# Kernel tuning notes

Hardware: AMD Instinct MI355X
Metric: run time of the kernel (lower is better)

## Reference

```python
import jax, jax.numpy as jnp
import numpy as np

POLY_DEGREE = 3


def setup_inputs() -> dict:
    key = jax.random.key(0)
    k1, k2, k3 = jax.random.split(key, 3)
    B, L, D = 8192, 16, 4096
    total = sum(L ** d for d in range(POLY_DEGREE + 1))  # 4369
    z = jax.random.normal(k1, (B, L), dtype=jnp.float32)
    W = jax.random.normal(k2, (total, D), dtype=jnp.float32) * 0.02
    b = jax.random.normal(k3, (D,), dtype=jnp.float32) * 0.02
    return {"z": z, "W": W, "b": b}


def poly_features(z):
    # Batched equivalent of per-sample torch.kron chain:
    # degree 0 -> [1]; degree k -> kron(deg_{k-1} feature, z) per sample.
    B = z.shape[0]
    feats = [jnp.ones((B, 1), dtype=z.dtype)]
    cur = z  # degree 1
    feats.append(cur)
    for _ in range(2, POLY_DEGREE + 1):
        # kron(out, latent): (i, j) -> out_i * latent_j
        cur = (cur[:, :, None] * z[:, None, :]).reshape(B, -1)
        feats.append(cur)
    return jnp.concatenate(feats, axis=1)  # [B, total_poly_terms]


def reference(z, W, b):
    x = poly_features(z)          # [B, T]
    return x @ W + b              # [B, data_dim]
```

## Files before the change

kernel.cpp:

```cpp
#include <hip/hip_runtime.h>
#include <hip/hip_bf16.h>

#define NDIM  4096
#define MROWS 8192
#define PREAL 969
#define KP    1024
#define NT    16
#define NWFOLD 1024

typedef unsigned short u16;
typedef __attribute__((ext_vector_type(8))) __bf16 bf16x8;
typedef __attribute__((ext_vector_type(8))) u16 u16x8;
typedef __attribute__((ext_vector_type(4))) float f32x4;

__device__ __forceinline__ u16 bf16rne(float f) {
  unsigned int u = __builtin_bit_cast(unsigned int, f);
  u += 0x7fffu + ((u >> 16) & 1u);
  return (u16)(u >> 16);
}

struct Tbl { int v[KP]; };
constexpr Tbl make_table() {
  Tbl t{};
  for (int p = 0; p < KP; ++p) t.v[p] = -1;
  int p = 0;
  t.v[p++] = (16 << 10) | (16 << 5) | 16;
  for (int i = 0; i < 16; ++i) t.v[p++] = (i << 10) | (16 << 5) | 16;
  for (int i = 0; i < 16; ++i)
    for (int j = i; j < 16; ++j) t.v[p++] = (i << 10) | (j << 5) | 16;
  for (int i = 0; i < 16; ++i)
    for (int j = i; j < 16; ++j)
      for (int k = j; k < 16; ++k) t.v[p++] = (i << 10) | (j << 5) | k;
  return t;
}
__device__ constexpr Tbl TBL = make_table();

__global__ void prep_kernel(const float* __restrict__ z, const float* __restrict__ W,
                            const float* __restrict__ bias,
                            u16* __restrict__ xb, u16* __restrict__ wfbt) {
  __shared__ float tile[64][65];
  __shared__ float zs[17];
  const int bx = blockIdx.x;
  const int tid = threadIdx.x;

  if (bx < NWFOLD) {
    const int p0 = (bx & 15) * 64;
    const int d0 = (bx >> 4) * 64;
    const int d4 = (tid & 15) * 4;
    const int rb = tid >> 4;
    const int dd = d0 + d4;
#pragma unroll
    for (int pp = 0; pp < 4; ++pp) {
      const int r = pp * 16 + rb;
      const int p = p0 + r;
      const int enc = TBL.v[p];
      f32x4 v = {0.f, 0.f, 0.f, 0.f};
      if (enc >= 0) {
        const int i = enc >> 10, j = (enc >> 5) & 31, k = enc & 31;
        if (k == 16) {
          if (j == 16) {
            if (i == 16) {
              v = *reinterpret_cast<const f32x4*>(W + dd);
              f32x4 bb = *reinterpret_cast<const f32x4*>(bias + dd);
              v.x += bb.x; v.y += bb.y; v.z += bb.z; v.w += bb.w;
            } else {
              v = *reinterpret_cast<const f32x4*>(W + (size_t)(1 + i) * NDIM + dd);
            }
          } else {
            v = *reinterpret_cast<const f32x4*>(W + (size_t)(17 + i * 16 + j) * NDIM + dd);
            if (i != j) {
              f32x4 w2 = *reinterpret_cast<const f32x4*>(W + (size_t)(17 + j * 16 + i) * NDIM + dd);
              v.x += w2.x; v.y += w2.y; v.z += w2.z; v.w += w2.w;
            }
          }
        } else {
          int rows[6];
          int nr = 0;
          rows[nr++] = 273 + i * 256 + j * 16 + k;
          if (i == j && j == k) {
          } else if (i == j) {
            rows[nr++] = 273 + i * 256 + k * 16 + i;
            rows[nr++] = 273 + k * 256 + i * 16 + i;
          } else if (j == k) {
            rows[nr++] = 273 + j * 256 + i * 16 + j;
            rows[nr++] = 273 + j * 256 + j * 16 + i;
          } else {
            rows[nr++] = 273 + i * 256 + k * 16 + j;
            rows[nr++] = 273 + j * 256 + i * 16 + k;
            rows[nr++] = 273 + j * 256 + k * 16 + i;
            rows[nr++] = 273 + k * 256 + i * 16 + j;
            rows[nr++] = 273 + k * 256 + j * 16 + i;
          }
          v = *reinterpret_cast<const f32x4*>(W + (size_t)rows[0] * NDIM + dd);
          for (int s = 1; s < nr; ++s) {
            f32x4 w2 = *reinterpret_cast<const f32x4*>(W + (size_t)rows[s] * NDIM + dd);
            v.x += w2.x; v.y += w2.y; v.z += w2.z; v.w += w2.w;
          }
        }
      }
#pragma unroll
      for (int jj = 0; jj < 4; ++jj) tile[r][d4 + jj] = v[jj];
    }
    __syncthreads();
#pragma unroll
    for (int round = 0; round < 2; ++round) {
      const int v = round * 256 + tid;
      const int d = v >> 3;
      const int tg = v & 7;
      u16x8 pack;
#pragma unroll
      for (int e = 0; e < 8; ++e) pack[e] = bf16rne(tile[tg * 8 + e][d]);
      *reinterpret_cast<u16x8*>(wfbt + (size_t)(d0 + d) * KP + p0 + tg * 8) = pack;
    }
  } else {
    const int row = bx - NWFOLD;
    if (tid < 16) zs[tid] = z[row * 16 + tid];
    if (tid == 16) zs[16] = 1.0f;
    __syncthreads();
    u16* xrow = xb + (size_t)row * KP;
    for (int g = tid; g < KP / 8; g += 256) {
      u16x8 pack;
#pragma unroll
      for (int e = 0; e < 8; ++e) {
        const int enc = TBL.v[g * 8 + e];
        float v = 0.0f;
        if (enc >= 0) v = zs[enc >> 10] * (zs[(enc >> 5) & 31] * zs[enc & 31]);
        pack[e] = bf16rne(v);
      }
      *reinterpret_cast<u16x8*>(xrow + g * 8) = pack;
    }
  }
}

#define GLOAD(gp, lp)                                                                     \
  __builtin_amdgcn_global_load_lds((const __attribute__((address_space(1))) unsigned int*)(gp), \
                                   (__attribute__((address_space(3))) unsigned int*)(lp), 16, 0, 0)

__device__ __forceinline__ void bar() {
  asm volatile("" ::: "memory");
  __builtin_amdgcn_s_barrier();
  asm volatile("" ::: "memory");
}

#define VM4 asm volatile("s_waitcnt vmcnt(4)" ::: "memory")

__global__ __launch_bounds__(512, 2) void gemm_kernel(const u16* __restrict__ xb,
                                                      const u16* __restrict__ wbt,
                                                      float* __restrict__ out) {
  __shared__ u16 lds[2 * 32768];

  const int bid  = blockIdx.x;
  const int xcd  = bid & 7;
  const int idx  = bid >> 3;
  const int mtl  = (idx >> 3) & 3;
  const int ntl  = (idx & 7) | ((idx >> 5) << 3);
  const int brow = (xcd * 4 + mtl) * 256;
  const int bcol = ntl * 256;

  const int tid  = threadIdx.x;
  const int lane = tid & 63;
  const int wid  = tid >> 6;
  const int wr   = wid >> 2;
  const int wc   = wid & 3;
  const int f    = lane & 15;
  const int q    = lane >> 4;
  const int f7   = f & 7;

  const int lr = lane >> 3;
  const int swzc = ((lane & 7) ^ lr) * 8;
  const u16* gA = xb  + (size_t)(brow + lr) * KP + swzc;
  const u16* gB = wbt + (size_t)(bcol + lr) * KP + swzc;
  const int aB0 = (wid >> 2) * 128 + (wid & 3) * 16;
  const int bB0 = (wid >> 1) * 64 + (wid & 1) * 16;

#define STGQ(gptr, region, rb, U) do {                                               \
    GLOAD((gptr) + (size_t)(rb) * KP + (U) * 64, (region) + (rb) * 64);              \
    GLOAD((gptr) + (size_t)((rb) + 8) * KP + (U) * 64, (region) + ((rb) + 8) * 64);  \
  } while (0)

#define RD_A(mi, kk) (*reinterpret_cast<const bf16x8*>(bufA + (wr * 128 + (mi) * 16 + f) * 64 + (((kk) * 4 + q) ^ f7) * 8))
#define RD_B(ni, kk) (*reinterpret_cast<const bf16x8*>(bufB + (wc * 64 + (ni) * 16 + f) * 64 + (((kk) * 4 + q) ^ f7) * 8))

#define RDA4(MOFF) do {                                                              \
    _Pragma("unroll") for (int _i = 0; _i < 4; ++_i) {                               \
      a_[_i][0] = RD_A((MOFF) + _i, 0); a_[_i][1] = RD_A((MOFF) + _i, 1); }          \
  } while (0)
#define RDB2(NOFF) do {                                                              \
    _Pragma("unroll") for (int _i = 0; _i < 2; ++_i) {                               \
      b_[(NOFF) + _i][0] = RD_B((NOFF) + _i, 0); b_[(NOFF) + _i][1] = RD_B((NOFF) + _i, 1); } \
  } while (0)

#define QUAD(MOFF, NOFF) do {                                                        \
    __builtin_amdgcn_s_setprio(1);                                                   \
    _Pragma("unroll") for (int _m = 0; _m < 4; ++_m)                                 \
    _Pragma("unroll") for (int _n = 0; _n < 2; ++_n)                                 \
    _Pragma("unroll") for (int _k = 0; _k < 2; ++_k)                                 \
      acc[(MOFF) + _m][(NOFF) + _n] = __builtin_amdgcn_mfma_f32_16x16x32_bf16(       \
          a_[_m][_k], b_[(NOFF) + _n][_k], acc[(MOFF) + _m][(NOFF) + _n], 0, 0, 0);  \
    __builtin_amdgcn_s_setprio(0);                                                   \
  } while (0)

#define TILE_BODY(cA, cB, nA, nB, U) do {                                            \
    bufA = (cA); bufB = (cB);                                                        \
    RDA4(0); RDB2(0); STGQ(gA, (nA), aB0, (U));                                      \
    bar(); QUAD(0, 0); VM4; bar();                                                   \
    RDB2(2);          STGQ(gB, (nB), bB0, (U));                                      \
    bar(); QUAD(0, 2); VM4; bar();                                                   \
    RDA4(4);          STGQ(gB, (nB), bB0 + 32, (U));                                 \
    bar(); QUAD(4, 2); bar();                                                        \
                      STGQ(gA, (nA), aB0 + 64, (U));                                 \
    bar(); QUAD(4, 0); VM4; bar();                                                   \
  } while (0)

  f32x4 acc[8][4] = {};
  bf16x8 a_[4][2], b_[4][2];
  const u16 *bufA, *bufB;

  u16* b0A = lds;            u16* b0B = lds + 16384;
  u16* b1A = lds + 32768;    u16* b1B = b1A + 16384;

  STGQ(gA, b0A, aB0, 0); STGQ(gB, b0B, bB0, 0);
  STGQ(gB, b0B, bB0 + 32, 0); STGQ(gA, b0A, aB0 + 64, 0);
  VM4; bar();

  for (int t = 0; t < NT; t += 2) {
    const int u2 = (t + 2 < NT) ? (t + 2) : 0;
    TILE_BODY(b0A, b0B, b1A, b1B, t + 1);
    TILE_BODY(b1A, b1B, b0A, b0B, u2);
  }
  asm volatile("s_waitcnt vmcnt(0)" ::: "memory");

  const int r0 = brow + wr * 128 + q * 4;
  const int c0 = bcol + wc * 64 + f;
#pragma unroll
  for (int mi = 0; mi < 8; ++mi)
#pragma unroll
    for (int ni = 0; ni < 4; ++ni) {
#pragma unroll
      for (int j = 0; j < 4; ++j)
        out[(size_t)(r0 + mi * 16 + j) * NDIM + (c0 + ni * 16)] = acc[mi][ni][j];
    }
}

__global__ void fallback_kernel(const float* __restrict__ z, const float* __restrict__ W,
                                const float* __restrict__ bias, float* __restrict__ out) {
  __shared__ float feat[4369];
  const int row = blockIdx.x;
  const int tid = threadIdx.x;
  for (int t = tid; t < 4369; t += 256) {
    float v;
    if (t == 0) v = 1.0f;
    else if (t < 17) v = z[row * 16 + t - 1];
    else if (t < 273) { int u = t - 17; v = z[row * 16 + (u >> 4)] * z[row * 16 + (u & 15)]; }
    else { int u = t - 273; v = z[row * 16 + ((u >> 8) & 15)] * (z[row * 16 + ((u >> 4) & 15)] * z[row * 16 + (u & 15)]); }
    feat[t] = v;
  }
  __syncthreads();
  float acc[16];
#pragma unroll
  for (int j = 0; j < 16; ++j) acc[j] = bias[tid + 256 * j];
  for (int t = 0; t < 4369; ++t) {
    const float fv = feat[t];
    const float* wrow = W + (size_t)t * NDIM;
#pragma unroll
    for (int j = 0; j < 16; ++j) acc[j] = fmaf(fv, wrow[tid + 256 * j], acc[j]);
  }
  float* orow = out + (size_t)row * NDIM;
#pragma unroll
  for (int j = 0; j < 16; ++j) orow[tid + 256 * j] = acc[j];
}

extern "C" void kernel_launch(void* const* d_in, const int* in_sizes, int n_in,
                              void* d_out, int out_size, void* d_ws, size_t ws_size,
                              hipStream_t stream) {
  const float* z = (const float*)d_in[0];
  const float* W = (const float*)d_in[1];
  const float* b = (const float*)d_in[2];
  float* out = (float*)d_out;

  const size_t xb_elems  = (size_t)MROWS * KP;
  const size_t wbt_elems = (size_t)NDIM * KP;
  const size_t need = (xb_elems + wbt_elems) * sizeof(u16);

  if (ws_size >= need) {
    u16* xb  = (u16*)d_ws;
    u16* wbt = xb + xb_elems;
    prep_kernel<<<NWFOLD + MROWS, 256, 0, stream>>>(z, W, b, xb, wbt);
    gemm_kernel<<<(MROWS / 256) * (NDIM / 256), 512, 0, stream>>>(xb, wbt, out);
  } else {
    fallback_kernel<<<MROWS, 256, 0, stream>>>(z, W, b, out);
  }
}
```

Measured before the change: 104.3 us.

## Process two N-tiles per block to overlap epilogue stores with next tile's prefetch

Each GEMM block now computes two adjacent 256-column output tiles in sequence, halving the grid to 256 blocks. The first K-loop's last stage prefetches the second tile's B data, so the pipeline keeps loading while the first tile's results are written. Output stores become nontemporal, and a dedicated last-tile body drains outstanding loads with smaller waitcnts. The grid shrinks to exactly one wave of 256 blocks, which cuts tail effects but lowers total parallelism and changes the XCD mapping.

```diff
diff --git a/kernel.cpp b/kernel.cpp
--- a/kernel.cpp
+++ b/kernel.cpp
@@ -143,6 +143,8 @@
 }
 
 #define VM4 asm volatile("s_waitcnt vmcnt(4)" ::: "memory")
+#define VM2 asm volatile("s_waitcnt vmcnt(2)" ::: "memory")
+#define VM0 asm volatile("s_waitcnt vmcnt(0)" ::: "memory")
 
 __global__ __launch_bounds__(512, 2) void gemm_kernel(const u16* __restrict__ xb,
                                                       const u16* __restrict__ wbt,
@@ -152,10 +154,10 @@
   const int bid  = blockIdx.x;
   const int xcd  = bid & 7;
   const int idx  = bid >> 3;
-  const int mtl  = (idx >> 3) & 3;
-  const int ntl  = (idx & 7) | ((idx >> 5) << 3);
+  const int mtl  = idx >> 3;
+  const int npr  = idx & 7;
   const int brow = (xcd * 4 + mtl) * 256;
-  const int bcol = ntl * 256;
+  const int bcol = npr * 512;
 
   const int tid  = threadIdx.x;
   const int lane = tid & 63;
@@ -168,8 +170,9 @@
 
   const int lr = lane >> 3;
   const int swzc = ((lane & 7) ^ lr) * 8;
-  const u16* gA = xb  + (size_t)(brow + lr) * KP + swzc;
-  const u16* gB = wbt + (size_t)(bcol + lr) * KP + swzc;
+  const u16* gA  = xb  + (size_t)(brow + lr) * KP + swzc;
+  const u16* gB  = wbt + (size_t)(bcol + lr) * KP + swzc;
+  const u16* gB2 = gB + (size_t)256 * KP;
   const int aB0 = (wid >> 2) * 128 + (wid & 3) * 16;
   const int bB0 = (wid >> 1) * 64 + (wid & 1) * 16;
 
@@ -200,18 +203,29 @@
     __builtin_amdgcn_s_setprio(0);                                                   \
   } while (0)
 
-#define TILE_BODY(cA, cB, nA, nB, U) do {                                            \
+#define TILE_BODY(cA, cB, nA, nB, U, GBP) do {                                       \
     bufA = (cA); bufB = (cB);                                                        \
     RDA4(0); RDB2(0); STGQ(gA, (nA), aB0, (U));                                      \
     bar(); QUAD(0, 0); VM4; bar();                                                   \
-    RDB2(2);          STGQ(gB, (nB), bB0, (U));                                      \
+    RDB2(2);          STGQ((GBP), (nB), bB0, (U));                                   \
     bar(); QUAD(0, 2); VM4; bar();                                                   \
-    RDA4(4);          STGQ(gB, (nB), bB0 + 32, (U));                                 \
+    RDA4(4);          STGQ((GBP), (nB), bB0 + 32, (U));                              \
     bar(); QUAD(4, 2); bar();                                                        \
                       STGQ(gA, (nA), aB0 + 64, (U));                                 \
     bar(); QUAD(4, 0); VM4; bar();                                                   \
   } while (0)
 
+#define TILE_LAST(cA, cB) do {                                                       \
+    bufA = (cA); bufB = (cB);                                                        \
+    RDA4(0); RDB2(0);                                                                \
+    bar(); QUAD(0, 0); VM2; bar();                                                   \
+    RDB2(2);                                                                         \
+    bar(); QUAD(0, 2); VM0; bar();                                                   \
+    RDA4(4);                                                                         \
+    bar(); QUAD(4, 2); bar();                                                        \
+    QUAD(4, 0);                                                                      \
+  } while (0)
+
   f32x4 acc[8][4] = {};
   bf16x8 a_[4][2], b_[4][2];
   const u16 *bufA, *bufB;
@@ -223,23 +237,54 @@
   STGQ(gB, b0B, bB0 + 32, 0); STGQ(gA, b0A, aB0 + 64, 0);
   VM4; bar();
 
-  for (int t = 0; t < NT; t += 2) {
-    const int u2 = (t + 2 < NT) ? (t + 2) : 0;
-    TILE_BODY(b0A, b0B, b1A, b1B, t + 1);
-    TILE_BODY(b1A, b1B, b0A, b0B, u2);
-  }
-  asm volatile("s_waitcnt vmcnt(0)" ::: "memory");
-
-  const int r0 = brow + wr * 128 + q * 4;
-  const int c0 = bcol + wc * 64 + f;
+  for (int t = 0; t < NT - 2; t += 2) {
+    TILE_BODY(b0A, b0B, b1A, b1B, t + 1, gB);
+    TILE_BODY(b1A, b1B, b0A, b0B, t + 2, gB);
+  }
+  TILE_BODY(b0A, b0B, b1A, b1B, NT - 1, gB);
+  TILE_BODY(b1A, b1B, b0A, b0B, 0, gB2);
+
+  {
+    const int r0 = brow + wr * 128 + q * 4;
+    const int c0 = bcol + wc * 64 + f;
+#pragma unroll
+    for (int mi = 0; mi < 8; ++mi)
+#pragma unroll
+      for (int ni = 0; ni < 4; ++ni)
+#pragma unroll
+        for (int j = 0; j < 4; ++j)
+          __builtin_nontemporal_store(acc[mi][ni][j],
+              &out[(size_t)(r0 + mi * 16 + j) * NDIM + (c0 + ni * 16)]);
+  }
+  VM0; bar();
+
 #pragma unroll
   for (int mi = 0; mi < 8; ++mi)
 #pragma unroll
     for (int ni = 0; ni < 4; ++ni) {
-#pragma unroll
-      for (int j = 0; j < 4; ++j)
-        out[(size_t)(r0 + mi * 16 + j) * NDIM + (c0 + ni * 16)] = acc[mi][ni][j];
+      const f32x4 z4 = {0.f, 0.f, 0.f, 0.f};
+      acc[mi][ni] = z4;
     }
+
+  for (int t = 0; t < NT - 2; t += 2) {
+    TILE_BODY(b0A, b0B, b1A, b1B, t + 1, gB2);
+    TILE_BODY(b1A, b1B, b0A, b0B, t + 2, gB2);
+  }
+  TILE_BODY(b0A, b0B, b1A, b1B, NT - 1, gB2);
+  TILE_LAST(b1A, b1B);
+
+  {
+    const int r0 = brow + wr * 128 + q * 4;
+    const int c0 = bcol + 256 + wc * 64 + f;
+#pragma unroll
+    for (int mi = 0; mi < 8; ++mi)
+#pragma unroll
+      for (int ni = 0; ni < 4; ++ni)
+#pragma unroll
+        for (int j = 0; j < 4; ++j)
+          __builtin_nontemporal_store(acc[mi][ni][j],
+              &out[(size_t)(r0 + mi * 16 + j) * NDIM + (c0 + ni * 16)]);
+  }
 }
 
 __global__ void fallback_kernel(const float* __restrict__ z, const float* __restrict__ W,
@@ -286,7 +331,7 @@
     u16* xb  = (u16*)d_ws;
     u16* wbt = xb + xb_elems;
     prep_kernel<<<NWFOLD + MROWS, 256, 0, stream>>>(z, W, b, xb, wbt);
-    gemm_kernel<<<(MROWS / 256) * (NDIM / 256), 512, 0, stream>>>(xb, wbt, out);
+    gemm_kernel<<<(MROWS / 256) * (NDIM / 512), 512, 0, stream>>>(xb, wbt, out);
   } else {
     fallback_kernel<<<MROWS, 256, 0, stream>>>(z, W, b, out);
   }
```

After: 139.8 us. 1.34x slower.

## Software-pipeline LDS fragment reads against MFMA quads across tile boundaries

Applied to the files above, without the earlier changes.

Restructures the GEMM main loop so each quad of MFMAs uses fragments loaded in the previous phase, while the next phase's LDS reads are issued first. The last quad of a tile is deferred into the next tile, with a peeled prologue and epilogue. About half the barriers per tile are removed. The goal is to hide LDS read latency behind matrix-core work, at the cost of more live fragment registers (double-buffered A and B) and possible spills at the 2-waves occupancy bound.

```diff
diff --git a/kernel.cpp b/kernel.cpp
--- a/kernel.cpp
+++ b/kernel.cpp
@@ -143,6 +143,8 @@
 }
 
 #define VM4 asm volatile("s_waitcnt vmcnt(4)" ::: "memory")
+#define VM1 asm volatile("s_waitcnt vmcnt(1)" ::: "memory")
+#define VM0 asm volatile("s_waitcnt vmcnt(0)" ::: "memory")
 
 __global__ __launch_bounds__(512, 2) void gemm_kernel(const u16* __restrict__ xb,
                                                       const u16* __restrict__ wbt,
@@ -181,39 +183,39 @@
 #define RD_A(mi, kk) (*reinterpret_cast<const bf16x8*>(bufA + (wr * 128 + (mi) * 16 + f) * 64 + (((kk) * 4 + q) ^ f7) * 8))
 #define RD_B(ni, kk) (*reinterpret_cast<const bf16x8*>(bufB + (wc * 64 + (ni) * 16 + f) * 64 + (((kk) * 4 + q) ^ f7) * 8))
 
-#define RDA4(MOFF) do {                                                              \
+#define RDA_TO(DST, MOFF) do {                                                       \
     _Pragma("unroll") for (int _i = 0; _i < 4; ++_i) {                               \
-      a_[_i][0] = RD_A((MOFF) + _i, 0); a_[_i][1] = RD_A((MOFF) + _i, 1); }          \
-  } while (0)
-#define RDB2(NOFF) do {                                                              \
+      DST[_i][0] = RD_A((MOFF) + _i, 0); DST[_i][1] = RD_A((MOFF) + _i, 1); }        \
+  } while (0)
+#define RDB_TO(DST, NOFF) do {                                                       \
     _Pragma("unroll") for (int _i = 0; _i < 2; ++_i) {                               \
-      b_[(NOFF) + _i][0] = RD_B((NOFF) + _i, 0); b_[(NOFF) + _i][1] = RD_B((NOFF) + _i, 1); } \
-  } while (0)
-
-#define QUAD(MOFF, NOFF) do {                                                        \
+      DST[_i][0] = RD_B((NOFF) + _i, 0); DST[_i][1] = RD_B((NOFF) + _i, 1); }        \
+  } while (0)
+
+#define QUADX(MOFF, NOFF, AF, BF) do {                                               \
     __builtin_amdgcn_s_setprio(1);                                                   \
     _Pragma("unroll") for (int _m = 0; _m < 4; ++_m)                                 \
     _Pragma("unroll") for (int _n = 0; _n < 2; ++_n)                                 \
     _Pragma("unroll") for (int _k = 0; _k < 2; ++_k)                                 \
       acc[(MOFF) + _m][(NOFF) + _n] = __builtin_amdgcn_mfma_f32_16x16x32_bf16(       \
-          a_[_m][_k], b_[(NOFF) + _n][_k], acc[(MOFF) + _m][(NOFF) + _n], 0, 0, 0);  \
+          AF[_m][_k], BF[_n][_k], acc[(MOFF) + _m][(NOFF) + _n], 0, 0, 0);           \
     __builtin_amdgcn_s_setprio(0);                                                   \
   } while (0)
 
-#define TILE_BODY(cA, cB, nA, nB, U) do {                                            \
+#define TILE_STD(cA, cB, nA, nB, U, B0R, B0U) do {                                   \
     bufA = (cA); bufB = (cB);                                                        \
-    RDA4(0); RDB2(0); STGQ(gA, (nA), aB0, (U));                                      \
-    bar(); QUAD(0, 0); VM4; bar();                                                   \
-    RDB2(2);          STGQ(gB, (nB), bB0, (U));                                      \
-    bar(); QUAD(0, 2); VM4; bar();                                                   \
-    RDA4(4);          STGQ(gB, (nB), bB0 + 32, (U));                                 \
-    bar(); QUAD(4, 2); bar();                                                        \
-                      STGQ(gA, (nA), aB0 + 64, (U));                                 \
-    bar(); QUAD(4, 0); VM4; bar();                                                   \
+    RDA_TO(A0, 0); RDB_TO(B0R, 0); STGQ(gA, (nA), aB0, (U));                         \
+    QUADX(4, 0, A1, B0U); VM4; bar();                                                \
+    RDB_TO(B1, 2);        STGQ(gB, (nB), bB0, (U));                                  \
+    QUADX(0, 0, A0, B0R); VM4; bar();                                                \
+    RDA_TO(A1, 4);        STGQ(gB, (nB), bB0 + 32, (U));                             \
+    QUADX(0, 2, A0, B1);  bar();                                                     \
+                          STGQ(gA, (nA), aB0 + 64, (U));                             \
+    QUADX(4, 2, A1, B1);  VM4; bar();                                                \
   } while (0)
 
   f32x4 acc[8][4] = {};
-  bf16x8 a_[4][2], b_[4][2];
+  bf16x8 A0[4][2], A1[4][2], B0a[2][2], B0b[2][2], B1[2][2];
   const u16 *bufA, *bufB;
 
   u16* b0A = lds;            u16* b0B = lds + 16384;
@@ -223,12 +225,30 @@
   STGQ(gB, b0B, bB0 + 32, 0); STGQ(gA, b0A, aB0 + 64, 0);
   VM4; bar();
 
-  for (int t = 0; t < NT; t += 2) {
-    const int u2 = (t + 2 < NT) ? (t + 2) : 0;
-    TILE_BODY(b0A, b0B, b1A, b1B, t + 1);
-    TILE_BODY(b1A, b1B, b0A, b0B, u2);
-  }
-  asm volatile("s_waitcnt vmcnt(0)" ::: "memory");
+  bufA = b0A; bufB = b0B;
+  RDA_TO(A0, 0); RDB_TO(B0a, 0); STGQ(gA, b1A, aB0, 1);
+  VM4; bar();
+  RDB_TO(B1, 2);        STGQ(gB, b1B, bB0, 1);
+  QUADX(0, 0, A0, B0a); VM4; bar();
+  RDA_TO(A1, 4);        STGQ(gB, b1B, bB0 + 32, 1);
+  QUADX(0, 2, A0, B1);  bar();
+                        STGQ(gA, b1A, aB0 + 64, 1);
+  QUADX(4, 2, A1, B1);  VM4; bar();
+
+  for (int t = 1; t < NT - 1; t += 2) {
+    TILE_STD(b1A, b1B, b0A, b0B, t + 1, B0b, B0a);
+    TILE_STD(b0A, b0B, b1A, b1B, t + 2, B0a, B0b);
+  }
+
+  bufA = b1A; bufB = b1B;
+  RDA_TO(A0, 0); RDB_TO(B0b, 0);
+  QUADX(4, 0, A1, B0a); VM1; bar();
+  RDB_TO(B1, 2);
+  QUADX(0, 0, A0, B0b); VM0; bar();
+  RDA_TO(A1, 4);
+  QUADX(0, 2, A0, B1);  bar();
+  QUADX(4, 2, A1, B1);
+  QUADX(4, 0, A1, B0b);
 
   const int r0 = brow + wr * 128 + q * 4;
   const int c0 = bcol + wc * 64 + f;
```

New measurement: 160.0 us. 1.53x slower.
